# Kernel tuning notes

Hardware: AMD Instinct MI355X
Metric: run time of the kernel (lower is better)

Reference implementation:

```python
import jax, jax.numpy as jnp
import numpy as np
from jax import lax

NUM_IM, ROIS = 32, 128          # images per batch, proposals per image
NUM_CLASSES, EMBED, OBJ_DIM = 151, 200, 2048
HALF_H = 256                    # per-direction LSTM hidden; bi concat -> 512
BN_EPS = 1e-5


def _lstm_dir(xs, wih, whh, b):
    # xs: [T, B, Din] -> hidden states [T, B, H]
    pre = jnp.einsum('tbd,dh->tbh', xs, wih) + b  # precompute input proj
    H = whh.shape[0]
    h0 = jnp.zeros((xs.shape[1], H), xs.dtype)
    def step(carry, pt):
        h, c = carry
        g = pt + h @ whh
        i, f, gg, o = jnp.split(g, 4, axis=-1)
        c = jax.nn.sigmoid(f) * c + jax.nn.sigmoid(i) * jnp.tanh(gg)
        h = jax.nn.sigmoid(o) * jnp.tanh(c)
        return (h, c), h
    _, hs = lax.scan(step, (h0, h0), pre)
    return hs


def _bilstm(x, wih, whh, b):
    # x: [B, T, D] -> [B, T, 2*HALF_H]; wih/whh/b carry both directions on axis 0
    xs = jnp.swapaxes(x, 0, 1)
    fwd = _lstm_dir(xs, wih[0], whh[0], b[0])
    bwd = _lstm_dir(xs[::-1], wih[1], whh[1], b[1])[::-1]
    return jnp.swapaxes(jnp.concatenate([fwd, bwd], -1), 0, 1)


def _context(feats, conf, params):
    # sort_rois: per-image descending confidence order, run 2-layer bi(tree)LSTM,
    # then scatter back with the inverse permutation (as in _sort_by_score).
    D = feats.shape[-1]
    f = feats.reshape(NUM_IM, ROIS, D)
    perm = jnp.argsort(-conf.reshape(NUM_IM, ROIS), axis=1)
    xs = jnp.take_along_axis(f, perm[..., None], axis=1)
    wih0, whh0, b0, wih1, whh1, b1 = params
    h = _bilstm(xs, wih0, whh0, b0)
    h = _bilstm(h, wih1, whh1, b1)
    inv = jnp.argsort(perm, axis=1)
    h = jnp.take_along_axis(h, inv[..., None], axis=1)
    return h.reshape(NUM_IM * ROIS, -1)


def setup_inputs() -> dict:
    key = jax.random.key(0)
    ks = jax.random.split(key, 24)
    N = NUM_IM * ROIS
    obj_fmaps = jax.random.normal(ks[0], (N, OBJ_DIM), jnp.float32)
    obj_logits = jax.random.normal(ks[1], (N, NUM_CLASSES), jnp.float32)
    xy = jax.random.uniform(ks[2], (N, 2), jnp.float32) * 500.0
    wh = jax.random.uniform(ks[3], (N, 2), jnp.float32) * 100.0 + 1.0
    boxes = jnp.concatenate([xy, xy + wh], axis=1)  # valid x1y1x2y2
    im_inds = jnp.repeat(jnp.arange(NUM_IM, dtype=jnp.int64), ROIS)
    w = lambda k, s: (jax.random.normal(k, s, jnp.float32) * 0.02)
    H4 = 4 * HALF_H
    D_obj, D_edge = OBJ_DIM + EMBED + 128, EMBED + 2 * HALF_H + OBJ_DIM
    return {
        'obj_fmaps': obj_fmaps, 'obj_logits': obj_logits, 'boxes': boxes,
        'im_inds': im_inds,
        'obj_embed_w': w(ks[4], (NUM_CLASSES, EMBED)),
        'obj_embed2_w': w(ks[5], (NUM_CLASSES, EMBED)),
        'bn_gamma': jnp.ones((4,), jnp.float32), 'bn_beta': jnp.zeros((4,), jnp.float32),
        'bn_mean': jnp.zeros((4,), jnp.float32), 'bn_var': jnp.ones((4,), jnp.float32),
        'pos_w': w(ks[6], (4, 128)), 'pos_b': jnp.zeros((128,), jnp.float32),
        'obj_wih0': w(ks[7], (2, D_obj, H4)), 'obj_whh0': w(ks[8], (2, HALF_H, H4)),
        'obj_b0': jnp.zeros((2, H4), jnp.float32),
        'obj_wih1': w(ks[9], (2, 2 * HALF_H, H4)), 'obj_whh1': w(ks[10], (2, HALF_H, H4)),
        'obj_b1': jnp.zeros((2, H4), jnp.float32),
        'edge_wih0': w(ks[11], (2, D_edge, H4)), 'edge_whh0': w(ks[12], (2, HALF_H, H4)),
        'edge_b0': jnp.zeros((2, H4), jnp.float32),
        'edge_wih1': w(ks[13], (2, 2 * HALF_H, H4)), 'edge_whh1': w(ks[14], (2, HALF_H, H4)),
        'edge_b1': jnp.zeros((2, H4), jnp.float32),
        'dec_w': w(ks[15], (D_obj + 2 * HALF_H, NUM_CLASSES)),
        'dec_b': jnp.zeros((NUM_CLASSES,), jnp.float32),
    }


def reference(obj_fmaps, obj_logits, boxes, im_inds, obj_embed_w, obj_embed2_w,
              bn_gamma, bn_beta, bn_mean, bn_var, pos_w, pos_b,
              obj_wih0, obj_whh0, obj_b0, obj_wih1, obj_whh1, obj_b1,
              edge_wih0, edge_whh0, edge_b0, edge_wih1, edge_whh1, edge_b1,
              dec_w, dec_b):
    probs = jax.nn.softmax(obj_logits, axis=-1)
    obj_embed = probs @ obj_embed_w                      # soft class embedding
    x1, y1, x2, y2 = boxes[:, 0], boxes[:, 1], boxes[:, 2], boxes[:, 3]
    cs = jnp.stack([(x1 + x2) * 0.5, (y1 + y2) * 0.5, x2 - x1, y2 - y1], axis=-1)
    csn = (cs - bn_mean) * lax.rsqrt(bn_var + BN_EPS) * bn_gamma + bn_beta
    pos = jax.nn.relu(csn @ pos_w + pos_b)               # BN(4)+Linear(4,128)+ReLU
    feats = jnp.concatenate([obj_fmaps, obj_embed, pos], axis=-1)  # [N, 2376]
    conf = jnp.max(probs[:, 1:], axis=-1)                # confidence (non-bg)
    enc = _context(feats, conf, (obj_wih0, obj_whh0, obj_b0,
                                 obj_wih1, obj_whh1, obj_b1))       # [N, 512]
    dec_in = jnp.concatenate([feats, enc], axis=-1)      # pass_in_obj_feats_to_decoder
    obj_dists = dec_in @ dec_w + dec_b                   # [N, 151]
    obj_preds = jnp.argmax(obj_dists[:, 1:], axis=-1) + 1
    edge_in = jnp.concatenate([obj_embed2_w[obj_preds], enc, obj_fmaps], axis=-1)
    edge_ctx = _context(edge_in, conf, (edge_wih0, edge_whh0, edge_b0,
                                        edge_wih1, edge_whh1, edge_b1))  # [N, 512]
    return jnp.concatenate([obj_dists, edge_ctx], axis=-1)  # [N, 663]
```

## Files before the change

### kernel.cpp

```cpp
#include <hip/hip_runtime.h>
#include <hip/hip_bf16.h>
#include <hip/hip_fp16.h>

typedef unsigned short u16;
typedef unsigned int u32;
typedef short s16x8 __attribute__((ext_vector_type(8)));
typedef float f32x4 __attribute__((ext_vector_type(4)));

#define FE_LD 2944
#define EDGE_LD 2816

static __device__ __forceinline__ int sdot4(u32 a, u32 b, int acc) {
  return __builtin_amdgcn_sdot4((int)a, (int)b, acc, false);
}
static __device__ __forceinline__ float fsig(float x) {
  return __builtin_amdgcn_rcpf(1.f + __expf(-x));
}
static __device__ __forceinline__ float ftanh(float x) {
  return 1.f - 2.f * __builtin_amdgcn_rcpf(1.f + __expf(2.f * x));
}

#define GLD_LDS16(gsrc, ldst) \
  __builtin_amdgcn_global_load_lds((const __attribute__((address_space(1))) void*)(gsrc), \
                                   (__attribute__((address_space(3))) void*)(ldst), 16, 0, 0)

__global__ __launch_bounds__(256) void gemm_kernel(
    const u16* __restrict__ A, int lda,
    const u16* __restrict__ B, int ldb,
    int K, int N,
    float* __restrict__ outF, __hip_bfloat16* __restrict__ outB, int ldc,
    const float* __restrict__ bias)
{
  __shared__ __align__(16) u16 As[128*64];
  __shared__ __align__(16) u16 Bs[128*64];
  const int tid = threadIdx.x;
  const int w = tid >> 6, lane = tid & 63;
  const int wm = w >> 1, wn = w & 1;
  const long bm = (long)blockIdx.x * 128;
  const long bn = (long)blockIdx.y * 128;
  f32x4 acc[4][4] = {};

  for (int k0 = 0; k0 < K; k0 += 64) {
    #pragma unroll
    for (int rr = 0; rr < 4; rr++) {
      int idx = rr * 256 + tid;
      int row = idx >> 3;
      int g   = idx & 7;
      int gs  = g ^ (row & 7);
      int ldst = (rr * 256 + (w << 6)) * 8;
      GLD_LDS16(A + (bm + row) * (long)lda + k0 + gs * 8, &As[ldst]);
      GLD_LDS16(B + (bn + row) * (long)ldb + k0 + gs * 8, &Bs[ldst]);
    }
    __syncthreads();
    #pragma unroll
    for (int kk = 0; kk < 2; kk++) {
      s16x8 af[4], bfr[4];
      #pragma unroll
      for (int i = 0; i < 4; i++) {
        int ra = wm * 64 + i * 16 + (lane & 15);
        int rb = wn * 64 + i * 16 + (lane & 15);
        int gg = kk * 4 + (lane >> 4);
        af[i]  = *(const s16x8*)&As[ra * 64 + ((gg ^ (ra & 7)) << 3)];
        bfr[i] = *(const s16x8*)&Bs[rb * 64 + ((gg ^ (rb & 7)) << 3)];
      }
      #pragma unroll
      for (int i = 0; i < 4; i++)
        #pragma unroll
        for (int j = 0; j < 4; j++)
          acc[i][j] = __builtin_amdgcn_mfma_f32_16x16x32_bf16(af[i], bfr[j], acc[i][j], 0, 0, 0);
    }
    __syncthreads();
  }

  #pragma unroll
  for (int i = 0; i < 4; i++)
    #pragma unroll
    for (int j = 0; j < 4; j++)
      #pragma unroll
      for (int v = 0; v < 4; v++) {
        long rr = bm + wm * 64 + i * 16 + (lane >> 4) * 4 + v;
        int  cc = (int)bn + wn * 64 + j * 16 + (lane & 15);
        if (cc < N) {
          float val = acc[i][j][v] + (bias ? bias[cc] : 0.f);
          if (outF) outF[rr * (long)ldc + cc] = val;
          else      outB[rr * (long)ldc + cc] = __float2bfloat16(val);
        }
      }
}

__global__ void transpose_cast(const float* __restrict__ src, __hip_bfloat16* __restrict__ dst,
                               int srcK, int srcN, int dstR, int dstC, int split, int split_off)
{
  __shared__ float tile[32][33];
  const int kt = blockIdx.x * 32, nt = blockIdx.y * 32;
  const int tx = threadIdx.x & 31, ty = threadIdx.x >> 5;
  for (int i = ty; i < 32; i += 8) {
    int k = kt + i;
    int srck = (k < split) ? (split_off + k) : (k - split);
    int n = nt + tx;
    tile[i][tx] = (srck < srcK && n < srcN) ? src[(size_t)srck * srcN + n] : 0.f;
  }
  __syncthreads();
  for (int i = ty; i < 32; i += 8) {
    int n = nt + i, k = kt + tx;
    if (n < dstR && k < dstC)
      dst[(size_t)n * dstC + k] = __float2bfloat16(tile[tx][i]);
  }
}

__global__ void pack_whh(const float* __restrict__ whh, u32* __restrict__ wreg,
                         u32* __restrict__ wlds, float* __restrict__ wsc)
{
  const int idx = blockIdx.x * 256 + threadIdx.x;
  const int d = idx >> 10, col = idx & 1023;
  const int c4 = col >> 8, j = col & 255;
  const float* s = whh + (size_t)d * 256 * 1024 + col;
  float mx = 0.f;
  for (int k = 0; k < 256; k++) mx = fmaxf(mx, fabsf(s[(size_t)k * 1024]));
  float inv = (mx > 0.f) ? 127.f / mx : 0.f;
  wsc[d * 1024 + col] = (mx > 0.f) ? mx / (127.f * 127.f) : 0.f;
  for (int kg = 0; kg < 4; kg++) {
    const int slot = kg * 256 + j;
    for (int w = 0; w < 16; w++) {
      u32 v = 0;
      #pragma unroll
      for (int b = 0; b < 4; b++) {
        int q = __float2int_rn(s[(size_t)(kg * 64 + 4 * w + b) * 1024] * inv);
        q = max(-127, min(127, q));
        v |= ((u32)(q & 0xff)) << (8 * b);
      }
      if (w < 8)
        wreg[(size_t)(d * 32 + c4 * 8 + w) * 1024 + slot] = v;
      else
        wlds[((size_t)(d * 8 + c4 * 2 + ((w - 8) >> 2)) * 1024 + slot) * 4 + ((w - 8) & 3)] = v;
    }
  }
}

__global__ void prep_kernel(
    const float* __restrict__ logits, const float* __restrict__ fmaps,
    const float* __restrict__ boxes,
    const float* __restrict__ bn_g, const float* __restrict__ bn_b,
    const float* __restrict__ bn_m, const float* __restrict__ bn_v,
    const float* __restrict__ pos_w, const float* __restrict__ pos_b,
    __hip_bfloat16* __restrict__ FE, __hip_bfloat16* __restrict__ probsb,
    float* __restrict__ conf)
{
  __shared__ float red[256];
  const int row = blockIdx.x, t = threadIdx.x;
  float v = (t < 151) ? logits[(size_t)row * 151 + t] : -3.0e38f;
  red[t] = v; __syncthreads();
  for (int s = 128; s > 0; s >>= 1) { if (t < s) red[t] = fmaxf(red[t], red[t + s]); __syncthreads(); }
  float mx = red[0]; __syncthreads();
  float p = (t < 151) ? expf(v - mx) : 0.f;
  red[t] = p; __syncthreads();
  for (int s = 128; s > 0; s >>= 1) { if (t < s) red[t] += red[t + s]; __syncthreads(); }
  float sum = red[0]; __syncthreads();
  p = p / sum;
  if (t < 192) probsb[(size_t)row * 192 + t] = __float2bfloat16((t < 151) ? p : 0.f);
  red[t] = (t >= 1 && t < 151) ? p : 0.f; __syncthreads();
  for (int s = 128; s > 0; s >>= 1) { if (t < s) red[t] = fmaxf(red[t], red[t + s]); __syncthreads(); }
  if (t == 0) conf[row] = red[0];

  if (t < 128) {
    float x1 = boxes[row * 4 + 0], y1 = boxes[row * 4 + 1];
    float x2 = boxes[row * 4 + 2], y2 = boxes[row * 4 + 3];
    float cs[4] = { (x1 + x2) * 0.5f, (y1 + y2) * 0.5f, x2 - x1, y2 - y1 };
    float a = pos_b[t];
    #pragma unroll
    for (int j = 0; j < 4; j++) {
      float cn = (cs[j] - bn_m[j]) * rsqrtf(bn_v[j] + 1e-5f) * bn_g[j] + bn_b[j];
      a += cn * pos_w[j * 128 + t];
    }
    FE[(size_t)row * FE_LD + 2760 + t] = __float2bfloat16(fmaxf(a, 0.f));
  }
  for (int c0 = t; c0 < 2048; c0 += 256)
    FE[(size_t)row * FE_LD + 512 + c0] = __float2bfloat16(fmaps[(size_t)row * 2048 + c0]);
}

__global__ void sort_kernel(const float* __restrict__ conf, int* __restrict__ perm)
{
  __shared__ float key[128];
  __shared__ int   idx[128];
  const int b = blockIdx.x, t = threadIdx.x;
  key[t] = conf[b * 128 + t]; idx[t] = t;
  __syncthreads();
  for (int k = 2; k <= 128; k <<= 1)
    for (int j = k >> 1; j > 0; j >>= 1) {
      int ixj = t ^ j;
      if (ixj > t) {
        bool up = (t & k) == 0;
        float ka = key[t], kb = key[ixj];
        int ia = idx[t], ib = idx[ixj];
        bool before = (ka > kb) || (ka == kb && ia < ib);
        if (before != up) { key[t] = kb; key[ixj] = ka; idx[t] = ib; idx[ixj] = ia; }
      }
      __syncthreads();
    }
  perm[b * 128 + t] = b * 128 + idx[t];
}

__global__ __launch_bounds__(1024) void rec_kernel(
    const float* __restrict__ P,
    const int* __restrict__ perm,
    const u32* __restrict__ wreg_g,
    const uint4* __restrict__ wlds_g,
    const float* __restrict__ wsc_g,
    int gatherPerm, int outPerm,
    __hip_bfloat16* __restrict__ out_bf, int out_ld,
    float* __restrict__ out_f32, int f32_ld, int f32_off)
{
  __shared__ __align__(16) uint4 wt4[8 * 1024];
  __shared__ __align__(16) int4 part[256 * 5];
  __shared__ __align__(16) u32 hq[64];
  __shared__ int prow_lds[128];
  const int tid = threadIdx.x;
  const int kg = tid >> 8;
  const int img = blockIdx.x & 31, dir = blockIdx.x >> 5;

  u32 wv[32];
  {
    const u32* rp = wreg_g + (size_t)dir * 32768 + tid;
    #pragma unroll
    for (int i = 0; i < 32; i++) wv[i] = rp[(size_t)i * 1024];
  }
  #pragma unroll
  for (int i = 0; i < 32; i++) asm volatile("" : "+v"(wv[i]));
  {
    const uint4* lp = wlds_g + (size_t)dir * 8192 + tid;
    #pragma unroll
    for (int q = 0; q < 8; q++) wt4[q * 1024 + tid] = lp[(size_t)q * 1024];
  }
  if (tid < 128) prow_lds[tid] = perm[img * 128 + tid];
  if (tid < 64) hq[tid] = 0;

  float sc0 = 0.f, sc1 = 0.f, sc2 = 0.f, sc3 = 0.f, cst = 0.f;
  if (tid < 256) {
    const float* sp = wsc_g + dir * 1024 + tid;
    sc0 = sp[0]; sc1 = sp[256]; sc2 = sp[512]; sc3 = sp[768];
  }
  __syncthreads();

  const uint4* hq4 = (const uint4*)hq;

  int st = dir ? 127 : 0;
  float p0 = 0.f, p1 = 0.f, p2 = 0.f, p3 = 0.f;
  if (tid < 256) {
    int prow0 = gatherPerm ? prow_lds[st] : (img * 128 + st);
    const float* pp = P + (size_t)prow0 * 2048 + dir * 1024 + tid;
    p0 = pp[0]; p1 = pp[256]; p2 = pp[512]; p3 = pp[768];
  }

  for (int t = 0; t < 128; t++) {
    float n0 = 0.f, n1 = 0.f, n2 = 0.f, n3 = 0.f;
    if (tid < 256 && t < 127) {
      int stn = dir ? (126 - t) : (t + 1);
      int prn = gatherPerm ? prow_lds[stn] : (img * 128 + stn);
      const float* pp = P + (size_t)prn * 2048 + dir * 1024 + tid;
      n0 = pp[0]; n1 = pp[256]; n2 = pp[512]; n3 = pp[768];
    }

    int a0 = 0, a1 = 0, a2 = 0, a3 = 0;
    #pragma unroll
    for (int hw = 0; hw < 2; hw++) {
      uint4 hv = hq4[kg * 4 + hw];
      #pragma unroll
      for (int s = 0; s < 4; s++) {
        u32 hp = (s == 0) ? hv.x : (s == 1) ? hv.y : (s == 2) ? hv.z : hv.w;
        int w = hw * 4 + s;
        a0 = sdot4(hp, wv[w], a0);
        a1 = sdot4(hp, wv[8 + w], a1);
        a2 = sdot4(hp, wv[16 + w], a2);
        a3 = sdot4(hp, wv[24 + w], a3);
      }
    }
    #pragma unroll
    for (int half = 0; half < 2; half++) {
      uint4 hv = hq4[kg * 4 + 2 + half];
      uint4 wl = wt4[(half) * 1024 + tid];
      a0 = sdot4(hv.x, wl.x, a0); a0 = sdot4(hv.y, wl.y, a0);
      a0 = sdot4(hv.z, wl.z, a0); a0 = sdot4(hv.w, wl.w, a0);
      wl = wt4[(2 + half) * 1024 + tid];
      a1 = sdot4(hv.x, wl.x, a1); a1 = sdot4(hv.y, wl.y, a1);
      a1 = sdot4(hv.z, wl.z, a1); a1 = sdot4(hv.w, wl.w, a1);
      wl = wt4[(4 + half) * 1024 + tid];
      a2 = sdot4(hv.x, wl.x, a2); a2 = sdot4(hv.y, wl.y, a2);
      a2 = sdot4(hv.z, wl.z, a2); a2 = sdot4(hv.w, wl.w, a2);
      wl = wt4[(6 + half) * 1024 + tid];
      a3 = sdot4(hv.x, wl.x, a3); a3 = sdot4(hv.y, wl.y, a3);
      a3 = sdot4(hv.z, wl.z, a3); a3 = sdot4(hv.w, wl.w, a3);
    }

    part[(tid & 255) * 5 + kg] = int4{a0, a1, a2, a3};
    __syncthreads();

    if (tid < 256) {
      int4 q0 = part[tid * 5 + 0], q1 = part[tid * 5 + 1];
      int4 q2 = part[tid * 5 + 2], q3 = part[tid * 5 + 3];
      float gi = (float)(q0.x + q1.x + q2.x + q3.x) * sc0 + p0;
      float gf = (float)(q0.y + q1.y + q2.y + q3.y) * sc1 + p1;
      float gg = (float)(q0.z + q1.z + q2.z + q3.z) * sc2 + p2;
      float go = (float)(q0.w + q1.w + q2.w + q3.w) * sc3 + p3;
      float si = fsig(gi), sf = fsig(gf), so = fsig(go);
      cst = sf * cst + si * ftanh(gg);
      float h = so * ftanh(cst);
      int qi = __float2int_rn(h * 127.f);
      ((signed char*)hq)[tid] = (signed char)qi;
      const int orow = outPerm ? prow_lds[st] : (img * 128 + st);
      if (out_bf)  out_bf[(size_t)orow * out_ld + dir * 256 + tid] = __float2bfloat16(h);
      if (out_f32) out_f32[(size_t)orow * f32_ld + f32_off + dir * 256 + tid] = h;
    }
    __syncthreads();
    p0 = n0; p1 = n1; p2 = n2; p3 = n3;
    st = dir ? (st - 1) : (st + 1);
  }
}

__global__ void argmax_kernel(const float* __restrict__ dists, int* __restrict__ preds)
{
  const int row = blockIdx.x * 4 + (threadIdx.x >> 6);
  const int lane = threadIdx.x & 63;
  float best = -3.4e38f; int bi = 1000;
  for (int cc = 1 + lane; cc < 151; cc += 64) {
    float v = dists[(size_t)row * 663 + cc];
    if (v > best) { best = v; bi = cc; }
  }
  for (int off = 32; off > 0; off >>= 1) {
    float ov = __shfl_down(best, off);
    int   oi = __shfl_down(bi, off);
    if (ov > best || (ov == best && oi < bi)) { best = ov; bi = oi; }
  }
  if (lane == 0) preds[row] = bi;
}

__global__ void edge_build(const int* __restrict__ preds,
                           const float* __restrict__ embed2,
                           const float* __restrict__ fmaps,
                           const __hip_bfloat16* __restrict__ FE,
                           __hip_bfloat16* __restrict__ EDGE)
{
  const int row = blockIdx.x, t = threadIdx.x;
  const int pr = preds[row];
  for (int c0 = t; c0 < 200; c0 += 256)
    EDGE[(size_t)row * EDGE_LD + c0] = __float2bfloat16(embed2[(size_t)pr * 200 + c0]);
  for (int c0 = t; c0 < 512; c0 += 256)
    EDGE[(size_t)row * EDGE_LD + 200 + c0] = FE[(size_t)row * FE_LD + c0];
  for (int c0 = t; c0 < 2048; c0 += 256)
    EDGE[(size_t)row * EDGE_LD + 712 + c0] = __float2bfloat16(fmaps[(size_t)row * 2048 + c0]);
}

extern "C" void kernel_launch(void* const* d_in, const int* in_sizes, int n_in,
                              void* d_out, int out_size, void* d_ws, size_t ws_size,
                              hipStream_t stream)
{
  const float* obj_fmaps    = (const float*)d_in[0];
  const float* obj_logits   = (const float*)d_in[1];
  const float* boxes        = (const float*)d_in[2];
  const float* obj_embed_w  = (const float*)d_in[4];
  const float* obj_embed2_w = (const float*)d_in[5];
  const float* bn_g = (const float*)d_in[6];
  const float* bn_b = (const float*)d_in[7];
  const float* bn_m = (const float*)d_in[8];
  const float* bn_v = (const float*)d_in[9];
  const float* pos_w = (const float*)d_in[10];
  const float* pos_b = (const float*)d_in[11];
  const float* obj_wih0 = (const float*)d_in[12];
  const float* obj_whh0 = (const float*)d_in[13];
  const float* obj_b0   = (const float*)d_in[14];
  const float* obj_wih1 = (const float*)d_in[15];
  const float* obj_whh1 = (const float*)d_in[16];
  const float* obj_b1   = (const float*)d_in[17];
  const float* edge_wih0 = (const float*)d_in[18];
  const float* edge_whh0 = (const float*)d_in[19];
  const float* edge_b0   = (const float*)d_in[20];
  const float* edge_wih1 = (const float*)d_in[21];
  const float* edge_whh1 = (const float*)d_in[22];
  const float* edge_b1   = (const float*)d_in[23];
  const float* dec_w = (const float*)d_in[24];
  const float* dec_b = (const float*)d_in[25];
  float* out = (float*)d_out;

  char* ws = (char*)d_ws;
  auto alloc = [&](size_t bytes) -> char* {
    char* p = ws; ws += (bytes + 255) & ~(size_t)255; return p;
  };
  __hip_bfloat16* FE     = (__hip_bfloat16*)alloc(4096ull * FE_LD * 2);
  __hip_bfloat16* EDGE   = (__hip_bfloat16*)alloc(4096ull * EDGE_LD * 2);
  float*          Pbuf   = (float*)alloc(4096ull * 2048 * 4);
  __hip_bfloat16* hseq   = (__hip_bfloat16*)alloc(4096ull * 512 * 2);
  __hip_bfloat16* probsb = (__hip_bfloat16*)alloc(4096ull * 192 * 2);
  __hip_bfloat16* wih0T  = (__hip_bfloat16*)alloc(2048ull * 2432 * 2);
  __hip_bfloat16* wih1T  = (__hip_bfloat16*)alloc(2048ull * 512 * 2);
  __hip_bfloat16* ewih0T = (__hip_bfloat16*)alloc(2048ull * 2816 * 2);
  __hip_bfloat16* ewih1T = (__hip_bfloat16*)alloc(2048ull * 512 * 2);
  __hip_bfloat16* embedT = (__hip_bfloat16*)alloc(256ull * 192 * 2);
  __hip_bfloat16* decT   = (__hip_bfloat16*)alloc(256ull * 2944 * 2);
  u32* whh0pk  = (u32*)alloc(133120ull * 4);
  u32* whh1pk  = (u32*)alloc(133120ull * 4);
  u32* ewhh0pk = (u32*)alloc(133120ull * 4);
  u32* ewhh1pk = (u32*)alloc(133120ull * 4);
  int*   perm  = (int*)alloc(4096 * 4);
  float* conf  = (float*)alloc(4096 * 4);
  int*   preds = (int*)alloc(4096 * 4);
  (void)in_sizes; (void)n_in; (void)out_size; (void)ws_size;

  auto tr = [&](const float* src, __hip_bfloat16* dst, int srcK, int srcN,
                int dstR, int dstC, int split, int soff) {
    dim3 g((dstC + 31) / 32, (dstR + 31) / 32);
    transpose_cast<<<g, dim3(256), 0, stream>>>(src, dst, srcK, srcN, dstR, dstC, split, soff);
  };
  for (int d = 0; d < 2; d++) {
    tr(obj_wih0 + (size_t)d * 2376 * 1024, wih0T + (size_t)d * 1024 * 2432, 2376, 1024, 1024, 2432, 0, 0);
    tr(obj_wih1 + (size_t)d * 512 * 1024,  wih1T + (size_t)d * 1024 * 512,  512, 1024, 1024, 512, 0, 0);
    tr(edge_wih0 + (size_t)d * 2760 * 1024, ewih0T + (size_t)d * 1024 * 2816, 2760, 1024, 1024, 2816, 0, 0);
    tr(edge_wih1 + (size_t)d * 512 * 1024,  ewih1T + (size_t)d * 1024 * 512,  512, 1024, 1024, 512, 0, 0);
  }
  tr(obj_embed_w, embedT, 151, 200, 256, 192, 0, 0);
  tr(dec_w, decT, 2888, 151, 256, 2944, 512, 2376);

  auto pk = [&](const float* whh, u32* dst) {
    pack_whh<<<dim3(8), dim3(256), 0, stream>>>(whh, dst, dst + 65536, (float*)(dst + 131072));
  };
  pk(obj_whh0, whh0pk); pk(obj_whh1, whh1pk); pk(edge_whh0, ewhh0pk); pk(edge_whh1, ewhh1pk);

  prep_kernel<<<dim3(4096), dim3(256), 0, stream>>>(
      obj_logits, obj_fmaps, boxes, bn_g, bn_b, bn_m, bn_v, pos_w, pos_b, FE, probsb, conf);
  sort_kernel<<<dim3(32), dim3(128), 0, stream>>>(conf, perm);

  auto gemm = [&](const void* A, int lda, const void* B, int ldb, int K, int N,
                  float* oF, __hip_bfloat16* oB, int ldc, const float* bias) {
    dim3 g(32, (N + 127) / 128);
    gemm_kernel<<<g, dim3(256), 0, stream>>>(
        (const u16*)A, lda, (const u16*)B, ldb, K, N, oF, oB, ldc, bias);
  };
  auto rec = [&](const float* P, const u32* wpk, int gat, int op,
                 __hip_bfloat16* ob, int old_, float* of, int fld, int foff) {
    rec_kernel<<<dim3(64), dim3(1024), 0, stream>>>(
        P, perm, wpk, (const uint4*)(wpk + 65536), (const float*)(wpk + 131072),
        gat, op, ob, old_, of, fld, foff);
  };

  gemm(probsb, 192, embedT, 192, 192, 200, nullptr, FE + 2560, FE_LD, nullptr);
  gemm((const u16*)FE + 512, FE_LD, wih0T, 2432, 2432, 2048, Pbuf, nullptr, 2048, obj_b0);
  rec(Pbuf, whh0pk, 1, 0, hseq, 512, nullptr, 0, 0);
  gemm(hseq, 512, wih1T, 512, 512, 2048, Pbuf, nullptr, 2048, obj_b1);
  rec(Pbuf, whh1pk, 0, 1, FE, FE_LD, nullptr, 0, 0);
  gemm(FE, FE_LD, decT, 2944, 2944, 151, out, nullptr, 663, dec_b);
  argmax_kernel<<<dim3(1024), dim3(256), 0, stream>>>(out, preds);
  edge_build<<<dim3(4096), dim3(256), 0, stream>>>(preds, obj_embed2_w, obj_fmaps, FE, EDGE);
  gemm(EDGE, EDGE_LD, ewih0T, 2816, 2816, 2048, Pbuf, nullptr, 2048, edge_b0);
  rec(Pbuf, ewhh0pk, 1, 0, hseq, 512, nullptr, 0, 0);
  gemm(hseq, 512, ewih1T, 512, 512, 2048, Pbuf, nullptr, 2048, edge_b1);
  rec(Pbuf, ewhh1pk, 0, 1, nullptr, 0, out, 663, 151);
}
```

Measured before the change: 1.007 ms.

## Store input projections in bf16 and move more recurrent weights into registers

The GEMM output P (the precomputed input projection) is now written as bf16 instead of fp32, which halves its write traffic and the per-step gather traffic in the recurrent kernel. The recurrent weight packing is also reworked so that 40 instead of 32 int8x4 words per thread are held in registers and only 6 instead of 8 uint4 slabs sit in LDS. This cuts LDS reads in the serial step loop. In exchange, precision of the input projection drops to bf16, and the higher register count may constrain the 1024-thread block.

```diff
diff --git a/kernel.cpp b/kernel.cpp
--- a/kernel.cpp
+++ b/kernel.cpp
@@ -119,6 +119,8 @@
   for (int k = 0; k < 256; k++) mx = fmaxf(mx, fabsf(s[(size_t)k * 1024]));
   float inv = (mx > 0.f) ? 127.f / mx : 0.f;
   wsc[d * 1024 + col] = (mx > 0.f) ? mx / (127.f * 127.f) : 0.f;
+  const int rc = (c4 < 2) ? 12 : 8;
+  const int rb = (c4 == 0) ? 0 : (c4 == 1) ? 12 : (c4 == 2) ? 24 : 32;
   for (int kg = 0; kg < 4; kg++) {
     const int slot = kg * 256 + j;
     for (int w = 0; w < 16; w++) {
@@ -129,10 +131,16 @@
         q = max(-127, min(127, q));
         v |= ((u32)(q & 0xff)) << (8 * b);
       }
-      if (w < 8)
-        wreg[(size_t)(d * 32 + c4 * 8 + w) * 1024 + slot] = v;
-      else
-        wlds[((size_t)(d * 8 + c4 * 2 + ((w - 8) >> 2)) * 1024 + slot) * 4 + ((w - 8) & 3)] = v;
+      if (w < rc) {
+        wreg[(size_t)(d * 40 + rb + w) * 1024 + slot] = v;
+      } else {
+        int qq, comp;
+        if (c4 == 0)      { qq = 0; comp = w - 12; }
+        else if (c4 == 1) { qq = 1; comp = w - 12; }
+        else if (c4 == 2) { qq = 2 + ((w - 8) >> 2); comp = (w - 8) & 3; }
+        else              { qq = 4 + ((w - 8) >> 2); comp = (w - 8) & 3; }
+        wlds[((size_t)(d * 6 + qq) * 1024 + slot) * 4 + comp] = v;
+      }
     }
   }
 }
@@ -201,7 +209,7 @@
 }
 
 __global__ __launch_bounds__(1024) void rec_kernel(
-    const float* __restrict__ P,
+    const __hip_bfloat16* __restrict__ P,
     const int* __restrict__ perm,
     const u32* __restrict__ wreg_g,
     const uint4* __restrict__ wlds_g,
@@ -210,7 +218,7 @@
     __hip_bfloat16* __restrict__ out_bf, int out_ld,
     float* __restrict__ out_f32, int f32_ld, int f32_off)
 {
-  __shared__ __align__(16) uint4 wt4[8 * 1024];
+  __shared__ __align__(16) uint4 wt4[6 * 1024];
   __shared__ __align__(16) int4 part[256 * 5];
   __shared__ __align__(16) u32 hq[64];
   __shared__ int prow_lds[128];
@@ -218,18 +226,18 @@
   const int kg = tid >> 8;
   const int img = blockIdx.x & 31, dir = blockIdx.x >> 5;
 
-  u32 wv[32];
+  u32 wv[40];
   {
-    const u32* rp = wreg_g + (size_t)dir * 32768 + tid;
-    #pragma unroll
-    for (int i = 0; i < 32; i++) wv[i] = rp[(size_t)i * 1024];
+    const u32* rp = wreg_g + (size_t)dir * 40960 + tid;
+    #pragma unroll
+    for (int i = 0; i < 40; i++) wv[i] = rp[(size_t)i * 1024];
   }
   #pragma unroll
-  for (int i = 0; i < 32; i++) asm volatile("" : "+v"(wv[i]));
+  for (int i = 0; i < 40; i++) asm volatile("" : "+v"(wv[i]));
   {
-    const uint4* lp = wlds_g + (size_t)dir * 8192 + tid;
-    #pragma unroll
-    for (int q = 0; q < 8; q++) wt4[q * 1024 + tid] = lp[(size_t)q * 1024];
+    const uint4* lp = wlds_g + (size_t)dir * 6144 + tid;
+    #pragma unroll
+    for (int q = 0; q < 6; q++) wt4[q * 1024 + tid] = lp[(size_t)q * 1024];
   }
   if (tid < 128) prow_lds[tid] = perm[img * 128 + tid];
   if (tid < 64) hq[tid] = 0;
@@ -247,8 +255,9 @@
   float p0 = 0.f, p1 = 0.f, p2 = 0.f, p3 = 0.f;
   if (tid < 256) {
     int prow0 = gatherPerm ? prow_lds[st] : (img * 128 + st);
-    const float* pp = P + (size_t)prow0 * 2048 + dir * 1024 + tid;
-    p0 = pp[0]; p1 = pp[256]; p2 = pp[512]; p3 = pp[768];
+    const __hip_bfloat16* pp = P + (size_t)prow0 * 2048 + dir * 1024 + tid;
+    p0 = __bfloat162float(pp[0]);   p1 = __bfloat162float(pp[256]);
+    p2 = __bfloat162float(pp[512]); p3 = __bfloat162float(pp[768]);
   }
 
   for (int t = 0; t < 128; t++) {
@@ -256,37 +265,59 @@
     if (tid < 256 && t < 127) {
       int stn = dir ? (126 - t) : (t + 1);
       int prn = gatherPerm ? prow_lds[stn] : (img * 128 + stn);
-      const float* pp = P + (size_t)prn * 2048 + dir * 1024 + tid;
-      n0 = pp[0]; n1 = pp[256]; n2 = pp[512]; n3 = pp[768];
+      const __hip_bfloat16* pp = P + (size_t)prn * 2048 + dir * 1024 + tid;
+      n0 = __bfloat162float(pp[0]);   n1 = __bfloat162float(pp[256]);
+      n2 = __bfloat162float(pp[512]); n3 = __bfloat162float(pp[768]);
     }
 
     int a0 = 0, a1 = 0, a2 = 0, a3 = 0;
-    #pragma unroll
-    for (int hw = 0; hw < 2; hw++) {
-      uint4 hv = hq4[kg * 4 + hw];
-      #pragma unroll
-      for (int s = 0; s < 4; s++) {
-        u32 hp = (s == 0) ? hv.x : (s == 1) ? hv.y : (s == 2) ? hv.z : hv.w;
-        int w = hw * 4 + s;
-        a0 = sdot4(hp, wv[w], a0);
-        a1 = sdot4(hp, wv[8 + w], a1);
-        a2 = sdot4(hp, wv[16 + w], a2);
-        a3 = sdot4(hp, wv[24 + w], a3);
-      }
-    }
-    #pragma unroll
-    for (int half = 0; half < 2; half++) {
-      uint4 hv = hq4[kg * 4 + 2 + half];
-      uint4 wl = wt4[(half) * 1024 + tid];
+    {
+      uint4 hv = hq4[kg * 4 + 0];
+      a0 = sdot4(hv.x, wv[0], a0);  a0 = sdot4(hv.y, wv[1], a0);
+      a0 = sdot4(hv.z, wv[2], a0);  a0 = sdot4(hv.w, wv[3], a0);
+      a1 = sdot4(hv.x, wv[12], a1); a1 = sdot4(hv.y, wv[13], a1);
+      a1 = sdot4(hv.z, wv[14], a1); a1 = sdot4(hv.w, wv[15], a1);
+      a2 = sdot4(hv.x, wv[24], a2); a2 = sdot4(hv.y, wv[25], a2);
+      a2 = sdot4(hv.z, wv[26], a2); a2 = sdot4(hv.w, wv[27], a2);
+      a3 = sdot4(hv.x, wv[32], a3); a3 = sdot4(hv.y, wv[33], a3);
+      a3 = sdot4(hv.z, wv[34], a3); a3 = sdot4(hv.w, wv[35], a3);
+    }
+    {
+      uint4 hv = hq4[kg * 4 + 1];
+      a0 = sdot4(hv.x, wv[4], a0);  a0 = sdot4(hv.y, wv[5], a0);
+      a0 = sdot4(hv.z, wv[6], a0);  a0 = sdot4(hv.w, wv[7], a0);
+      a1 = sdot4(hv.x, wv[16], a1); a1 = sdot4(hv.y, wv[17], a1);
+      a1 = sdot4(hv.z, wv[18], a1); a1 = sdot4(hv.w, wv[19], a1);
+      a2 = sdot4(hv.x, wv[28], a2); a2 = sdot4(hv.y, wv[29], a2);
+      a2 = sdot4(hv.z, wv[30], a2); a2 = sdot4(hv.w, wv[31], a2);
+      a3 = sdot4(hv.x, wv[36], a3); a3 = sdot4(hv.y, wv[37], a3);
+      a3 = sdot4(hv.z, wv[38], a3); a3 = sdot4(hv.w, wv[39], a3);
+    }
+    {
+      uint4 hv = hq4[kg * 4 + 2];
+      a0 = sdot4(hv.x, wv[8], a0);  a0 = sdot4(hv.y, wv[9], a0);
+      a0 = sdot4(hv.z, wv[10], a0); a0 = sdot4(hv.w, wv[11], a0);
+      a1 = sdot4(hv.x, wv[20], a1); a1 = sdot4(hv.y, wv[21], a1);
+      a1 = sdot4(hv.z, wv[22], a1); a1 = sdot4(hv.w, wv[23], a1);
+      uint4 wl = wt4[2 * 1024 + tid];
+      a2 = sdot4(hv.x, wl.x, a2); a2 = sdot4(hv.y, wl.y, a2);
+      a2 = sdot4(hv.z, wl.z, a2); a2 = sdot4(hv.w, wl.w, a2);
+      wl = wt4[4 * 1024 + tid];
+      a3 = sdot4(hv.x, wl.x, a3); a3 = sdot4(hv.y, wl.y, a3);
+      a3 = sdot4(hv.z, wl.z, a3); a3 = sdot4(hv.w, wl.w, a3);
+    }
+    {
+      uint4 hv = hq4[kg * 4 + 3];
+      uint4 wl = wt4[0 * 1024 + tid];
       a0 = sdot4(hv.x, wl.x, a0); a0 = sdot4(hv.y, wl.y, a0);
       a0 = sdot4(hv.z, wl.z, a0); a0 = sdot4(hv.w, wl.w, a0);
-      wl = wt4[(2 + half) * 1024 + tid];
+      wl = wt4[1 * 1024 + tid];
       a1 = sdot4(hv.x, wl.x, a1); a1 = sdot4(hv.y, wl.y, a1);
       a1 = sdot4(hv.z, wl.z, a1); a1 = sdot4(hv.w, wl.w, a1);
-      wl = wt4[(4 + half) * 1024 + tid];
+      wl = wt4[3 * 1024 + tid];
       a2 = sdot4(hv.x, wl.x, a2); a2 = sdot4(hv.y, wl.y, a2);
       a2 = sdot4(hv.z, wl.z, a2); a2 = sdot4(hv.w, wl.w, a2);
-      wl = wt4[(6 + half) * 1024 + tid];
+      wl = wt4[5 * 1024 + tid];
       a3 = sdot4(hv.x, wl.x, a3); a3 = sdot4(hv.y, wl.y, a3);
       a3 = sdot4(hv.z, wl.z, a3); a3 = sdot4(hv.w, wl.w, a3);
     }
@@ -386,7 +417,7 @@
   };
   __hip_bfloat16* FE     = (__hip_bfloat16*)alloc(4096ull * FE_LD * 2);
   __hip_bfloat16* EDGE   = (__hip_bfloat16*)alloc(4096ull * EDGE_LD * 2);
-  float*          Pbuf   = (float*)alloc(4096ull * 2048 * 4);
+  __hip_bfloat16* Pbuf   = (__hip_bfloat16*)alloc(4096ull * 2048 * 2);
   __hip_bfloat16* hseq   = (__hip_bfloat16*)alloc(4096ull * 512 * 2);
   __hip_bfloat16* probsb = (__hip_bfloat16*)alloc(4096ull * 192 * 2);
   __hip_bfloat16* wih0T  = (__hip_bfloat16*)alloc(2048ull * 2432 * 2);
@@ -419,7 +450,7 @@
   tr(dec_w, decT, 2888, 151, 256, 2944, 512, 2376);
 
   auto pk = [&](const float* whh, u32* dst) {
-    pack_whh<<<dim3(8), dim3(256), 0, stream>>>(whh, dst, dst + 65536, (float*)(dst + 131072));
+    pack_whh<<<dim3(8), dim3(256), 0, stream>>>(whh, dst, dst + 81920, (float*)(dst + 131072));
   };
   pk(obj_whh0, whh0pk); pk(obj_whh1, whh1pk); pk(edge_whh0, ewhh0pk); pk(edge_whh1, ewhh1pk);
 
@@ -433,23 +464,23 @@
     gemm_kernel<<<g, dim3(256), 0, stream>>>(
         (const u16*)A, lda, (const u16*)B, ldb, K, N, oF, oB, ldc, bias);
   };
-  auto rec = [&](const float* P, const u32* wpk, int gat, int op,
+  auto rec = [&](const __hip_bfloat16* P, const u32* wpk, int gat, int op,
                  __hip_bfloat16* ob, int old_, float* of, int fld, int foff) {
     rec_kernel<<<dim3(64), dim3(1024), 0, stream>>>(
-        P, perm, wpk, (const uint4*)(wpk + 65536), (const float*)(wpk + 131072),
+        P, perm, wpk, (const uint4*)(wpk + 81920), (const float*)(wpk + 131072),
         gat, op, ob, old_, of, fld, foff);
   };
 
   gemm(probsb, 192, embedT, 192, 192, 200, nullptr, FE + 2560, FE_LD, nullptr);
-  gemm((const u16*)FE + 512, FE_LD, wih0T, 2432, 2432, 2048, Pbuf, nullptr, 2048, obj_b0);
+  gemm((const u16*)FE + 512, FE_LD, wih0T, 2432, 2432, 2048, nullptr, Pbuf, 2048, obj_b0);
   rec(Pbuf, whh0pk, 1, 0, hseq, 512, nullptr, 0, 0);
-  gemm(hseq, 512, wih1T, 512, 512, 2048, Pbuf, nullptr, 2048, obj_b1);
+  gemm(hseq, 512, wih1T, 512, 512, 2048, nullptr, Pbuf, 2048, obj_b1);
   rec(Pbuf, whh1pk, 0, 1, FE, FE_LD, nullptr, 0, 0);
   gemm(FE, FE_LD, decT, 2944, 2944, 151, out, nullptr, 663, dec_b);
   argmax_kernel<<<dim3(1024), dim3(256), 0, stream>>>(out, preds);
   edge_build<<<dim3(4096), dim3(256), 0, stream>>>(preds, obj_embed2_w, obj_fmaps, FE, EDGE);
-  gemm(EDGE, EDGE_LD, ewih0T, 2816, 2816, 2048, Pbuf, nullptr, 2048, edge_b0);
+  gemm(EDGE, EDGE_LD, ewih0T, 2816, 2816, 2048, nullptr, Pbuf, 2048, edge_b0);
   rec(Pbuf, ewhh0pk, 1, 0, hseq, 512, nullptr, 0, 0);
-  gemm(hseq, 512, ewih1T, 512, 512, 2048, Pbuf, nullptr, 2048, edge_b1);
+  gemm(hseq, 512, ewih1T, 512, 512, 2048, nullptr, Pbuf, 2048, edge_b1);
   rec(Pbuf, ewhh1pk, 0, 1, nullptr, 0, out, 663, 151);
 }
```

New measurement: 1.080 ms. 1.07x slower.
